# Kernel optimization log

Measured on AMD Instinct MI355X. Metric: run time of the kernel, lower is better.

Reference implementation:

```python
import jax, jax.numpy as jnp
import numpy as np

LOTRI2MAT = np.array([[0, 1, 3], [1, 2, 4], [3, 4, 5]])  # lower-tri 6-vec -> symmetric 3x3
MAT2LOTRI_I = np.array([0, 1, 1, 2, 2, 2])
MAT2LOTRI_J = np.array([0, 0, 1, 0, 1, 2])


def trilinear_warp_border(img, ddf):
    """MONAI Warp(mode='bilinear', padding_mode='border', align_corners=True).
    img: (B,C,H,W,D), ddf: (B,3,H,W,D) displacement in voxel units.
    Samples img at x + ddf(x), clamping coords to the volume (border padding).
    """
    B, C, H, W, D = img.shape
    base = jnp.stack(
        jnp.meshgrid(jnp.arange(H), jnp.arange(W), jnp.arange(D), indexing='ij'),
        axis=0,
    ).astype(img.dtype)  # (3,H,W,D)
    coords = ddf + base[None]  # (B,3,H,W,D)
    x = jnp.clip(coords[:, 0], 0.0, H - 1)
    y = jnp.clip(coords[:, 1], 0.0, W - 1)
    z = jnp.clip(coords[:, 2], 0.0, D - 1)

    x0f, y0f, z0f = jnp.floor(x), jnp.floor(y), jnp.floor(z)
    fx, fy, fz = x - x0f, y - y0f, z - z0f
    x0 = jnp.clip(x0f.astype(jnp.int32), 0, H - 1)
    y0 = jnp.clip(y0f.astype(jnp.int32), 0, W - 1)
    z0 = jnp.clip(z0f.astype(jnp.int32), 0, D - 1)
    x1 = jnp.minimum(x0 + 1, H - 1)
    y1 = jnp.minimum(y0 + 1, W - 1)
    z1 = jnp.minimum(z0 + 1, D - 1)

    def gather(img_b, xi, yi, zi):
        flat = (xi * W + yi) * D + zi  # (H,W,D)
        return img_b.reshape(C, -1)[:, flat.reshape(-1)].reshape(C, H, W, D)

    g = jax.vmap(gather)  # over batch

    out = jnp.zeros_like(img)
    for xi, wx in ((x0, 1.0 - fx), (x1, fx)):
        for yi, wy in ((y0, 1.0 - fy), (y1, fy)):
            for zi, wz in ((z0, 1.0 - fz), (z1, fz)):
                out = out + g(img, xi, yi, zi) * (wx * wy * wz)[:, None]
    return out


def jacobian_of_ddf(ddf):
    """J = I + du/dx via central differences (one-sided at boundaries).
    ddf: (B,3,H,W,D) -> (B,H,W,D,3,3) with J[...,i,j] = d u_i / d x_j + delta_ij."""
    grads = jnp.gradient(ddf, axis=(2, 3, 4))  # list over j of (B,3,H,W,D)
    J = jnp.stack(grads, axis=2)  # (B,3(i),3(j),H,W,D)
    J = J + jnp.eye(3, dtype=ddf.dtype)[None, :, :, None, None, None]
    return jnp.transpose(J, (0, 3, 4, 5, 1, 2))  # (B,H,W,D,3,3)


def setup_inputs() -> dict:
    key = jax.random.key(0)
    k1, k2 = jax.random.split(key)
    dti = jax.random.normal(k1, (2, 6, 64, 64, 64), dtype=jnp.float32)
    ddf = jax.random.normal(k2, (2, 3, 64, 64, 64), dtype=jnp.float32)
    return {"dti": dti, "ddf": ddf}


def reference(dti, ddf):
    b, _, h, w, d = dti.shape
    # 1) trilinear warp of the 6-channel lower-tri DTI
    dti_warped = trilinear_warp_border(dti, ddf)  # (B,6,H,W,D)
    # 2) lower-tri -> full symmetric 3x3, spatial-last
    M = dti_warped[:, LOTRI2MAT]                      # (B,3,3,H,W,D)
    M = jnp.transpose(M, (0, 3, 4, 5, 1, 2))          # (B,H,W,D,3,3)
    # 3) Jacobian of the deformation and its polar-decomposition rotation (finite strain)
    J = jacobian_of_ddf(ddf)                          # (B,H,W,D,3,3)
    U, _, Vh = jnp.linalg.svd(J, full_matrices=False)
    R = jnp.matmul(U, Vh)                             # orthogonal factor of J
    # 4) rotate tensors: R^T M R
    out = jnp.einsum('...ji,...jk,...kl->...il', R, M, R)
    # 5) back to lower-tri channel-first form
    out = jnp.transpose(out, (0, 4, 5, 1, 2, 3))      # (B,3,3,H,W,D)
    return out[:, MAT2LOTRI_I, MAT2LOTRI_J]           # (B,6,H,W,D)
```

## Files before the change

kernel.cpp:

```cpp
#include <hip/hip_runtime.h>

#define NVOX 262144
#define TOTAL (2 * NVOX)

typedef float f2u __attribute__((ext_vector_type(2), aligned(4)));

__global__ void zero_count(int* __restrict__ bad) {
    if (threadIdx.x == 0) bad[0] = 0;
}

__global__ __launch_bounds__(256)
void warp_main(const float* __restrict__ dti,
               const float* __restrict__ ddf,
               float* __restrict__ out,
               int* __restrict__ bad, int max_bad)
{
    const int idx = blockIdx.x * 256 + threadIdx.x;
    const int b = idx >> 18;
    const int r = idx & (NVOX - 1);
    const int x = r >> 12;
    const int y = (r >> 6) & 63;
    const int z = r & 63;

    const float* db = ddf + (size_t)b * 3 * NVOX;

    const float ux = db[r];
    const float uy = db[NVOX + r];
    const float uz = db[2 * NVOX + r];

    const float cx = fminf(fmaxf((float)x + ux, 0.0f), 63.0f);
    const float cy = fminf(fmaxf((float)y + uy, 0.0f), 63.0f);
    const float cz = fminf(fmaxf((float)z + uz, 0.0f), 63.0f);
    const float fx0 = floorf(cx), fy0 = floorf(cy), fz0 = floorf(cz);
    const float fx = cx - fx0, fy = cy - fy0, fz = cz - fz0;
    const int x0 = (int)fx0, y0 = (int)fy0, z0 = (int)fz0;
    const int x1 = min(x0 + 1, 63), y1 = min(y0 + 1, 63);

    const float gx = 1.0f - fx, gy = 1.0f - fy, gz = 1.0f - fz;
    const float q00 = gx * gy, q01 = gx * fy, q10 = fx * gy, q11 = fx * fy;

    const bool ztop = (z0 == 63);
    const int zb = ztop ? 62 : z0;
    const int p00 = (x0 * 64 + y0) * 64 + zb, p01 = (x0 * 64 + y1) * 64 + zb;
    const int p10 = (x1 * 64 + y0) * 64 + zb, p11 = (x1 * 64 + y1) * 64 + zb;

    const float* tb = dti + (size_t)b * 6 * NVOX;
    float m[6];
#pragma unroll
    for (int c = 0; c < 6; ++c) {
        const float* tc = tb + c * NVOX;
        const f2u v00 = *(const f2u*)(tc + p00);
        const f2u v01 = *(const f2u*)(tc + p01);
        const f2u v10 = *(const f2u*)(tc + p10);
        const f2u v11 = *(const f2u*)(tc + p11);
        const float l00 = (ztop ? v00.y : v00.x) * gz + v00.y * fz;
        const float l01 = (ztop ? v01.y : v01.x) * gz + v01.y * fz;
        const float l10 = (ztop ? v10.y : v10.x) * gz + v10.y * fz;
        const float l11 = (ztop ? v11.y : v11.x) * gz + v11.y * fz;
        m[c] = q00 * l00 + q01 * l01 + q10 * l10 + q11 * l11;
    }

    const int xm = max(x - 1, 0), xp = min(x + 1, 63);
    const int ym = max(y - 1, 0), yp = min(y + 1, 63);
    const int zm = max(z - 1, 0), zp = min(z + 1, 63);
    const float sx = (xp - xm == 2) ? 0.5f : 1.0f;
    const float sy = (yp - ym == 2) ? 0.5f : 1.0f;
    const float sz = (zp - zm == 2) ? 0.5f : 1.0f;

    float P[3][3];
#pragma unroll
    for (int i = 0; i < 3; ++i) {
        const float* ui = db + i * NVOX;
        const float ctr = (i == 0) ? ux : (i == 1) ? uy : uz;
        P[i][0] = (ui[(xp * 64 + y) * 64 + z] - ui[(xm * 64 + y) * 64 + z]) * sx
                + (i == 0 ? 1.0f : 0.0f);
        P[i][1] = (ui[(x * 64 + yp) * 64 + z] - ui[(x * 64 + ym) * 64 + z]) * sy
                + (i == 1 ? 1.0f : 0.0f);
        P[i][2] = (__shfl(ctr, zp) - __shfl(ctr, zm)) * sz + (i == 2 ? 1.0f : 0.0f);
    }

    float cond_est = 0.0f;
#pragma unroll
    for (int it = 0; it < 6; ++it) {
        const float C00 = P[1][1] * P[2][2] - P[1][2] * P[2][1];
        const float C01 = P[1][2] * P[2][0] - P[1][0] * P[2][2];
        const float C02 = P[1][0] * P[2][1] - P[1][1] * P[2][0];
        const float C10 = P[0][2] * P[2][1] - P[0][1] * P[2][2];
        const float C11 = P[0][0] * P[2][2] - P[0][2] * P[2][0];
        const float C12 = P[0][1] * P[2][0] - P[0][0] * P[2][1];
        const float C20 = P[0][1] * P[1][2] - P[0][2] * P[1][1];
        const float C21 = P[0][2] * P[1][0] - P[0][0] * P[1][2];
        const float C22 = P[0][0] * P[1][1] - P[0][1] * P[1][0];
        const float det = P[0][0] * C00 + P[0][1] * C01 + P[0][2] * C02;

        const float n2 = P[0][0]*P[0][0] + P[0][1]*P[0][1] + P[0][2]*P[0][2]
                       + P[1][0]*P[1][0] + P[1][1]*P[1][1] + P[1][2]*P[1][2]
                       + P[2][0]*P[2][0] + P[2][1]*P[2][1] + P[2][2]*P[2][2];
        const float a2 = C00*C00 + C01*C01 + C02*C02
                       + C10*C10 + C11*C11 + C12*C12
                       + C20*C20 + C21*C21 + C22*C22;

        const float ad = fmaxf(fabsf(det), 1e-30f);
        if (it == 0) cond_est = sqrtf(n2 * a2) / ad;

        const float t  = fmaxf(sqrtf(a2 / n2), 1e-20f);
        const float sg = (det < 0.0f) ? -1.0f : 1.0f;
        const float c1 = 0.5f * sqrtf(t / ad);
        const float c2 = 0.5f * sg / sqrtf(t * ad);

        P[0][0] = c1 * P[0][0] + c2 * C00;  P[0][1] = c1 * P[0][1] + c2 * C01;  P[0][2] = c1 * P[0][2] + c2 * C02;
        P[1][0] = c1 * P[1][0] + c2 * C10;  P[1][1] = c1 * P[1][1] + c2 * C11;  P[1][2] = c1 * P[1][2] + c2 * C12;
        P[2][0] = c1 * P[2][0] + c2 * C20;  P[2][1] = c1 * P[2][1] + c2 * C21;  P[2][2] = c1 * P[2][2] + c2 * C22;
    }

    const float M3[3][3] = {{m[0], m[1], m[3]},
                            {m[1], m[2], m[4]},
                            {m[3], m[4], m[5]}};
    float T[3][3];
#pragma unroll
    for (int i = 0; i < 3; ++i)
#pragma unroll
        for (int j = 0; j < 3; ++j)
            T[i][j] = P[0][i] * M3[0][j] + P[1][i] * M3[1][j] + P[2][i] * M3[2][j];

    float A[3][3];
#pragma unroll
    for (int i = 0; i < 3; ++i)
#pragma unroll
        for (int j = 0; j < 3; ++j)
            A[i][j] = T[i][0] * P[0][j] + T[i][1] * P[1][j] + T[i][2] * P[2][j];

    float* ob = out + (size_t)b * 6 * NVOX;
    ob[0 * NVOX + r] = A[0][0];
    ob[1 * NVOX + r] = A[1][0];
    ob[2 * NVOX + r] = A[1][1];
    ob[3 * NVOX + r] = A[2][0];
    ob[4 * NVOX + r] = A[2][1];
    ob[5 * NVOX + r] = A[2][2];

    if (cond_est > 1e4f) {
        const int slot = atomicAdd(bad, 1);
        if (slot < max_bad) bad[1 + slot] = idx;
    }
}

__global__ __launch_bounds__(256)
void rescue(const float* __restrict__ dti,
            const float* __restrict__ ddf,
            float* __restrict__ out,
            const int* __restrict__ bad, int max_bad)
{
    const int n = min(bad[0], max_bad);
    for (int k = blockIdx.x * 256 + threadIdx.x; k < n; k += 4 * 256) {
        const int idx = bad[1 + k];
        const int b = idx >> 18;
        const int r = idx & (NVOX - 1);
        const int x = r >> 12;
        const int y = (r >> 6) & 63;
        const int z = r & 63;

        const float* db = ddf + (size_t)b * 3 * NVOX;

        const float cx = fminf(fmaxf((float)x + db[r], 0.0f), 63.0f);
        const float cy = fminf(fmaxf((float)y + db[NVOX + r], 0.0f), 63.0f);
        const float cz = fminf(fmaxf((float)z + db[2 * NVOX + r], 0.0f), 63.0f);
        const float fx0 = floorf(cx), fy0 = floorf(cy), fz0 = floorf(cz);
        const float fx = cx - fx0, fy = cy - fy0, fz = cz - fz0;
        const int x0 = (int)fx0, y0 = (int)fy0, z0 = (int)fz0;
        const int x1 = min(x0 + 1, 63), y1 = min(y0 + 1, 63), z1 = min(z0 + 1, 63);
        const float gx = 1.0f - fx, gy = 1.0f - fy, gz = 1.0f - fz;
        const float w000 = gx*gy*gz, w001 = gx*gy*fz, w010 = gx*fy*gz, w011 = gx*fy*fz;
        const float w100 = fx*gy*gz, w101 = fx*gy*fz, w110 = fx*fy*gz, w111 = fx*fy*fz;
        const int o000 = (x0*64+y0)*64+z0, o001 = (x0*64+y0)*64+z1;
        const int o010 = (x0*64+y1)*64+z0, o011 = (x0*64+y1)*64+z1;
        const int o100 = (x1*64+y0)*64+z0, o101 = (x1*64+y0)*64+z1;
        const int o110 = (x1*64+y1)*64+z0, o111 = (x1*64+y1)*64+z1;

        const float* tb = dti + (size_t)b * 6 * NVOX;
        float m[6];
        for (int c = 0; c < 6; ++c) {
            const float* tc = tb + c * NVOX;
            m[c] = w000*tc[o000] + w001*tc[o001] + w010*tc[o010] + w011*tc[o011]
                 + w100*tc[o100] + w101*tc[o101] + w110*tc[o110] + w111*tc[o111];
        }

        const int xm = max(x-1,0), xp = min(x+1,63);
        const int ym = max(y-1,0), yp = min(y+1,63);
        const int zm = max(z-1,0), zp = min(z+1,63);
        const double sx = (xp-xm==2)?0.5:1.0, sy = (yp-ym==2)?0.5:1.0, sz = (zp-zm==2)?0.5:1.0;
        double X[3][3];
        for (int i = 0; i < 3; ++i) {
            const float* ui = db + i * NVOX;
            X[i][0] = ((double)ui[(xp*64+y)*64+z] - (double)ui[(xm*64+y)*64+z]) * sx + (i==0?1.0:0.0);
            X[i][1] = ((double)ui[(x*64+yp)*64+z] - (double)ui[(x*64+ym)*64+z]) * sy + (i==1?1.0:0.0);
            X[i][2] = ((double)ui[(x*64+y)*64+zp] - (double)ui[(x*64+y)*64+zm]) * sz + (i==2?1.0:0.0);
        }

        for (int it = 0; it < 14; ++it) {
            double mx = 0.0;
            for (int i = 0; i < 3; ++i)
                for (int j = 0; j < 3; ++j) mx = fmax(mx, fabs(X[i][j]));
            const double s = 1.0 / fmax(mx, 1e-300);
            for (int i = 0; i < 3; ++i)
                for (int j = 0; j < 3; ++j) X[i][j] *= s;

            const double C00 = X[1][1]*X[2][2] - X[1][2]*X[2][1];
            const double C01 = X[1][2]*X[2][0] - X[1][0]*X[2][2];
            const double C02 = X[1][0]*X[2][1] - X[1][1]*X[2][0];
            const double C10 = X[0][2]*X[2][1] - X[0][1]*X[2][2];
            const double C11 = X[0][0]*X[2][2] - X[0][2]*X[2][0];
            const double C12 = X[0][1]*X[2][0] - X[0][0]*X[2][1];
            const double C20 = X[0][1]*X[1][2] - X[0][2]*X[1][1];
            const double C21 = X[0][2]*X[1][0] - X[0][0]*X[1][2];
            const double C22 = X[0][0]*X[1][1] - X[0][1]*X[1][0];
            const double det = X[0][0]*C00 + X[0][1]*C01 + X[0][2]*C02;
            const double n2 = X[0][0]*X[0][0]+X[0][1]*X[0][1]+X[0][2]*X[0][2]
                            + X[1][0]*X[1][0]+X[1][1]*X[1][1]+X[1][2]*X[1][2]
                            + X[2][0]*X[2][0]+X[2][1]*X[2][1]+X[2][2]*X[2][2];
            const double a2 = C00*C00+C01*C01+C02*C02 + C10*C10+C11*C11+C12*C12
                            + C20*C20+C21*C21+C22*C22;
            const double t  = fmax(sqrt(a2 / n2), 1e-150);
            const double ad = fmax(fabs(det), 1e-280);
            const double sg = (det < 0.0) ? -1.0 : 1.0;
            const double c1 = 0.5 * sqrt(t / ad);
            const double c2 = 0.5 * sg / sqrt(t * ad);
            X[0][0]=c1*X[0][0]+c2*C00; X[0][1]=c1*X[0][1]+c2*C01; X[0][2]=c1*X[0][2]+c2*C02;
            X[1][0]=c1*X[1][0]+c2*C10; X[1][1]=c1*X[1][1]+c2*C11; X[1][2]=c1*X[1][2]+c2*C12;
            X[2][0]=c1*X[2][0]+c2*C20; X[2][1]=c1*X[2][1]+c2*C21; X[2][2]=c1*X[2][2]+c2*C22;
        }

        const double M3[3][3] = {{(double)m[0], (double)m[1], (double)m[3]},
                                 {(double)m[1], (double)m[2], (double)m[4]},
                                 {(double)m[3], (double)m[4], (double)m[5]}};
        double T[3][3], A[3][3];
        for (int i = 0; i < 3; ++i)
            for (int j = 0; j < 3; ++j)
                T[i][j] = X[0][i]*M3[0][j] + X[1][i]*M3[1][j] + X[2][i]*M3[2][j];
        for (int i = 0; i < 3; ++i)
            for (int j = 0; j < 3; ++j)
                A[i][j] = T[i][0]*X[0][j] + T[i][1]*X[1][j] + T[i][2]*X[2][j];

        float* ob = out + (size_t)b * 6 * NVOX;
        ob[0 * NVOX + r] = (float)A[0][0];
        ob[1 * NVOX + r] = (float)A[1][0];
        ob[2 * NVOX + r] = (float)A[1][1];
        ob[3 * NVOX + r] = (float)A[2][0];
        ob[4 * NVOX + r] = (float)A[2][1];
        ob[5 * NVOX + r] = (float)A[2][2];
    }
}

extern "C" void kernel_launch(void* const* d_in, const int* in_sizes, int n_in,
                              void* d_out, int out_size, void* d_ws, size_t ws_size,
                              hipStream_t stream) {
    const float* dti = (const float*)d_in[0];
    const float* ddf = (const float*)d_in[1];
    float* out = (float*)d_out;
    int* bad = (int*)d_ws;
    const int max_bad = (int)min((size_t)8192, ws_size / 4 - 1);

    zero_count<<<1, 64, 0, stream>>>(bad);
    warp_main<<<TOTAL / 256, 256, 0, stream>>>(dti, ddf, out, bad, max_bad);
    rescue<<<4, 256, 0, stream>>>(dti, ddf, out, bad, max_bad);
}
```

Measured before the change: 108.1 us.

## Replace atomic bad-list rescue with full-grid recheck kernel and fast math intrinsics

Drops the zero-count kernel and the atomic append of ill-conditioned voxels in the main kernel. A second full-grid kernel instead recomputes the Jacobian and condition estimate for every voxel and runs the double-precision polar iteration only where the estimate exceeds the threshold. The main kernel's Newton step now uses hardware rcp/rsq/sqrt intrinsics instead of IEEE divides and square roots. The trade is one fewer launch and no atomics, against a second full pass that rereads ddf for all 524K voxels, plus slightly less accurate float math.

After: 102.2 us. 1.06x faster.

```diff
diff --git a/kernel.cpp b/kernel.cpp
--- a/kernel.cpp
+++ b/kernel.cpp
@@ -4,16 +4,11 @@
 #define TOTAL (2 * NVOX)
 
 typedef float f2u __attribute__((ext_vector_type(2), aligned(4)));
-
-__global__ void zero_count(int* __restrict__ bad) {
-    if (threadIdx.x == 0) bad[0] = 0;
-}
 
 __global__ __launch_bounds__(256)
 void warp_main(const float* __restrict__ dti,
                const float* __restrict__ ddf,
-               float* __restrict__ out,
-               int* __restrict__ bad, int max_bad)
+               float* __restrict__ out)
 {
     const int idx = blockIdx.x * 256 + threadIdx.x;
     const int b = idx >> 18;
@@ -79,7 +74,6 @@
         P[i][2] = (__shfl(ctr, zp) - __shfl(ctr, zm)) * sz + (i == 2 ? 1.0f : 0.0f);
     }
 
-    float cond_est = 0.0f;
 #pragma unroll
     for (int it = 0; it < 6; ++it) {
         const float C00 = P[1][1] * P[2][2] - P[1][2] * P[2][1];
@@ -101,12 +95,11 @@
                        + C20*C20 + C21*C21 + C22*C22;
 
         const float ad = fmaxf(fabsf(det), 1e-30f);
-        if (it == 0) cond_est = sqrtf(n2 * a2) / ad;
-
-        const float t  = fmaxf(sqrtf(a2 / n2), 1e-20f);
+        const float t  = fmaxf(__builtin_amdgcn_sqrtf(a2 * __builtin_amdgcn_rcpf(n2)), 1e-20f);
         const float sg = (det < 0.0f) ? -1.0f : 1.0f;
-        const float c1 = 0.5f * sqrtf(t / ad);
-        const float c2 = 0.5f * sg / sqrtf(t * ad);
+        const float rt = __builtin_amdgcn_rsqf(t * ad);
+        const float c1 = 0.5f * t * rt;
+        const float c2 = 0.5f * sg * rt;
 
         P[0][0] = c1 * P[0][0] + c2 * C00;  P[0][1] = c1 * P[0][1] + c2 * C01;  P[0][2] = c1 * P[0][2] + c2 * C02;
         P[1][0] = c1 * P[1][0] + c2 * C10;  P[1][1] = c1 * P[1][1] + c2 * C11;  P[1][2] = c1 * P[1][2] + c2 * C12;
@@ -137,117 +130,140 @@
     ob[3 * NVOX + r] = A[2][0];
     ob[4 * NVOX + r] = A[2][1];
     ob[5 * NVOX + r] = A[2][2];
-
-    if (cond_est > 1e4f) {
-        const int slot = atomicAdd(bad, 1);
-        if (slot < max_bad) bad[1 + slot] = idx;
-    }
 }
 
 __global__ __launch_bounds__(256)
-void rescue(const float* __restrict__ dti,
-            const float* __restrict__ ddf,
-            float* __restrict__ out,
-            const int* __restrict__ bad, int max_bad)
+void rescue_all(const float* __restrict__ dti,
+                const float* __restrict__ ddf,
+                float* __restrict__ out)
 {
-    const int n = min(bad[0], max_bad);
-    for (int k = blockIdx.x * 256 + threadIdx.x; k < n; k += 4 * 256) {
-        const int idx = bad[1 + k];
-        const int b = idx >> 18;
-        const int r = idx & (NVOX - 1);
-        const int x = r >> 12;
-        const int y = (r >> 6) & 63;
-        const int z = r & 63;
-
-        const float* db = ddf + (size_t)b * 3 * NVOX;
-
-        const float cx = fminf(fmaxf((float)x + db[r], 0.0f), 63.0f);
-        const float cy = fminf(fmaxf((float)y + db[NVOX + r], 0.0f), 63.0f);
-        const float cz = fminf(fmaxf((float)z + db[2 * NVOX + r], 0.0f), 63.0f);
-        const float fx0 = floorf(cx), fy0 = floorf(cy), fz0 = floorf(cz);
-        const float fx = cx - fx0, fy = cy - fy0, fz = cz - fz0;
-        const int x0 = (int)fx0, y0 = (int)fy0, z0 = (int)fz0;
-        const int x1 = min(x0 + 1, 63), y1 = min(y0 + 1, 63), z1 = min(z0 + 1, 63);
-        const float gx = 1.0f - fx, gy = 1.0f - fy, gz = 1.0f - fz;
-        const float w000 = gx*gy*gz, w001 = gx*gy*fz, w010 = gx*fy*gz, w011 = gx*fy*fz;
-        const float w100 = fx*gy*gz, w101 = fx*gy*fz, w110 = fx*fy*gz, w111 = fx*fy*fz;
-        const int o000 = (x0*64+y0)*64+z0, o001 = (x0*64+y0)*64+z1;
-        const int o010 = (x0*64+y1)*64+z0, o011 = (x0*64+y1)*64+z1;
-        const int o100 = (x1*64+y0)*64+z0, o101 = (x1*64+y0)*64+z1;
-        const int o110 = (x1*64+y1)*64+z0, o111 = (x1*64+y1)*64+z1;
-
-        const float* tb = dti + (size_t)b * 6 * NVOX;
-        float m[6];
-        for (int c = 0; c < 6; ++c) {
-            const float* tc = tb + c * NVOX;
-            m[c] = w000*tc[o000] + w001*tc[o001] + w010*tc[o010] + w011*tc[o011]
-                 + w100*tc[o100] + w101*tc[o101] + w110*tc[o110] + w111*tc[o111];
-        }
-
-        const int xm = max(x-1,0), xp = min(x+1,63);
-        const int ym = max(y-1,0), yp = min(y+1,63);
-        const int zm = max(z-1,0), zp = min(z+1,63);
-        const double sx = (xp-xm==2)?0.5:1.0, sy = (yp-ym==2)?0.5:1.0, sz = (zp-zm==2)?0.5:1.0;
-        double X[3][3];
-        for (int i = 0; i < 3; ++i) {
-            const float* ui = db + i * NVOX;
-            X[i][0] = ((double)ui[(xp*64+y)*64+z] - (double)ui[(xm*64+y)*64+z]) * sx + (i==0?1.0:0.0);
-            X[i][1] = ((double)ui[(x*64+yp)*64+z] - (double)ui[(x*64+ym)*64+z]) * sy + (i==1?1.0:0.0);
-            X[i][2] = ((double)ui[(x*64+y)*64+zp] - (double)ui[(x*64+y)*64+zm]) * sz + (i==2?1.0:0.0);
-        }
-
-        for (int it = 0; it < 14; ++it) {
-            double mx = 0.0;
-            for (int i = 0; i < 3; ++i)
-                for (int j = 0; j < 3; ++j) mx = fmax(mx, fabs(X[i][j]));
-            const double s = 1.0 / fmax(mx, 1e-300);
-            for (int i = 0; i < 3; ++i)
-                for (int j = 0; j < 3; ++j) X[i][j] *= s;
-
-            const double C00 = X[1][1]*X[2][2] - X[1][2]*X[2][1];
-            const double C01 = X[1][2]*X[2][0] - X[1][0]*X[2][2];
-            const double C02 = X[1][0]*X[2][1] - X[1][1]*X[2][0];
-            const double C10 = X[0][2]*X[2][1] - X[0][1]*X[2][2];
-            const double C11 = X[0][0]*X[2][2] - X[0][2]*X[2][0];
-            const double C12 = X[0][1]*X[2][0] - X[0][0]*X[2][1];
-            const double C20 = X[0][1]*X[1][2] - X[0][2]*X[1][1];
-            const double C21 = X[0][2]*X[1][0] - X[0][0]*X[1][2];
-            const double C22 = X[0][0]*X[1][1] - X[0][1]*X[1][0];
-            const double det = X[0][0]*C00 + X[0][1]*C01 + X[0][2]*C02;
-            const double n2 = X[0][0]*X[0][0]+X[0][1]*X[0][1]+X[0][2]*X[0][2]
-                            + X[1][0]*X[1][0]+X[1][1]*X[1][1]+X[1][2]*X[1][2]
-                            + X[2][0]*X[2][0]+X[2][1]*X[2][1]+X[2][2]*X[2][2];
-            const double a2 = C00*C00+C01*C01+C02*C02 + C10*C10+C11*C11+C12*C12
-                            + C20*C20+C21*C21+C22*C22;
-            const double t  = fmax(sqrt(a2 / n2), 1e-150);
-            const double ad = fmax(fabs(det), 1e-280);
-            const double sg = (det < 0.0) ? -1.0 : 1.0;
-            const double c1 = 0.5 * sqrt(t / ad);
-            const double c2 = 0.5 * sg / sqrt(t * ad);
-            X[0][0]=c1*X[0][0]+c2*C00; X[0][1]=c1*X[0][1]+c2*C01; X[0][2]=c1*X[0][2]+c2*C02;
-            X[1][0]=c1*X[1][0]+c2*C10; X[1][1]=c1*X[1][1]+c2*C11; X[1][2]=c1*X[1][2]+c2*C12;
-            X[2][0]=c1*X[2][0]+c2*C20; X[2][1]=c1*X[2][1]+c2*C21; X[2][2]=c1*X[2][2]+c2*C22;
-        }
-
-        const double M3[3][3] = {{(double)m[0], (double)m[1], (double)m[3]},
-                                 {(double)m[1], (double)m[2], (double)m[4]},
-                                 {(double)m[3], (double)m[4], (double)m[5]}};
-        double T[3][3], A[3][3];
+    const int idx = blockIdx.x * 256 + threadIdx.x;
+    const int b = idx >> 18;
+    const int r = idx & (NVOX - 1);
+    const int x = r >> 12;
+    const int y = (r >> 6) & 63;
+    const int z = r & 63;
+
+    const float* db = ddf + (size_t)b * 3 * NVOX;
+
+    const int xm = max(x - 1, 0), xp = min(x + 1, 63);
+    const int ym = max(y - 1, 0), yp = min(y + 1, 63);
+    const int zm = max(z - 1, 0), zp = min(z + 1, 63);
+    const float sx = (xp - xm == 2) ? 0.5f : 1.0f;
+    const float sy = (yp - ym == 2) ? 0.5f : 1.0f;
+    const float sz = (zp - zm == 2) ? 0.5f : 1.0f;
+
+    float Jm[3][3];
+#pragma unroll
+    for (int i = 0; i < 3; ++i) {
+        const float* ui = db + i * NVOX;
+        Jm[i][0] = (ui[(xp * 64 + y) * 64 + z] - ui[(xm * 64 + y) * 64 + z]) * sx
+                 + (i == 0 ? 1.0f : 0.0f);
+        Jm[i][1] = (ui[(x * 64 + yp) * 64 + z] - ui[(x * 64 + ym) * 64 + z]) * sy
+                 + (i == 1 ? 1.0f : 0.0f);
+        Jm[i][2] = (ui[(x * 64 + y) * 64 + zp] - ui[(x * 64 + y) * 64 + zm]) * sz
+                 + (i == 2 ? 1.0f : 0.0f);
+    }
+
+    {
+        const float C00 = Jm[1][1]*Jm[2][2] - Jm[1][2]*Jm[2][1];
+        const float C01 = Jm[1][2]*Jm[2][0] - Jm[1][0]*Jm[2][2];
+        const float C02 = Jm[1][0]*Jm[2][1] - Jm[1][1]*Jm[2][0];
+        const float C10 = Jm[0][2]*Jm[2][1] - Jm[0][1]*Jm[2][2];
+        const float C11 = Jm[0][0]*Jm[2][2] - Jm[0][2]*Jm[2][0];
+        const float C12 = Jm[0][1]*Jm[2][0] - Jm[0][0]*Jm[2][1];
+        const float C20 = Jm[0][1]*Jm[1][2] - Jm[0][2]*Jm[1][1];
+        const float C21 = Jm[0][2]*Jm[1][0] - Jm[0][0]*Jm[1][2];
+        const float C22 = Jm[0][0]*Jm[1][1] - Jm[0][1]*Jm[1][0];
+        const float det = Jm[0][0]*C00 + Jm[0][1]*C01 + Jm[0][2]*C02;
+        const float n2 = Jm[0][0]*Jm[0][0]+Jm[0][1]*Jm[0][1]+Jm[0][2]*Jm[0][2]
+                       + Jm[1][0]*Jm[1][0]+Jm[1][1]*Jm[1][1]+Jm[1][2]*Jm[1][2]
+                       + Jm[2][0]*Jm[2][0]+Jm[2][1]*Jm[2][1]+Jm[2][2]*Jm[2][2];
+        const float a2 = C00*C00+C01*C01+C02*C02 + C10*C10+C11*C11+C12*C12
+                       + C20*C20+C21*C21+C22*C22;
+        const float ad = fmaxf(fabsf(det), 1e-30f);
+        const float ce = sqrtf(n2 * a2);
+        if (!(ce > 1e4f * ad)) return;
+    }
+
+    const float cx = fminf(fmaxf((float)x + db[r], 0.0f), 63.0f);
+    const float cy = fminf(fmaxf((float)y + db[NVOX + r], 0.0f), 63.0f);
+    const float cz = fminf(fmaxf((float)z + db[2 * NVOX + r], 0.0f), 63.0f);
+    const float fx0 = floorf(cx), fy0 = floorf(cy), fz0 = floorf(cz);
+    const float fx = cx - fx0, fy = cy - fy0, fz = cz - fz0;
+    const int x0 = (int)fx0, y0 = (int)fy0, z0 = (int)fz0;
+    const int x1 = min(x0 + 1, 63), y1 = min(y0 + 1, 63), z1 = min(z0 + 1, 63);
+    const float gx = 1.0f - fx, gy = 1.0f - fy, gz = 1.0f - fz;
+    const float w000 = gx*gy*gz, w001 = gx*gy*fz, w010 = gx*fy*gz, w011 = gx*fy*fz;
+    const float w100 = fx*gy*gz, w101 = fx*gy*fz, w110 = fx*fy*gz, w111 = fx*fy*fz;
+    const int o000 = (x0*64+y0)*64+z0, o001 = (x0*64+y0)*64+z1;
+    const int o010 = (x0*64+y1)*64+z0, o011 = (x0*64+y1)*64+z1;
+    const int o100 = (x1*64+y0)*64+z0, o101 = (x1*64+y0)*64+z1;
+    const int o110 = (x1*64+y1)*64+z0, o111 = (x1*64+y1)*64+z1;
+
+    const float* tb = dti + (size_t)b * 6 * NVOX;
+    float m[6];
+    for (int c = 0; c < 6; ++c) {
+        const float* tc = tb + c * NVOX;
+        m[c] = w000*tc[o000] + w001*tc[o001] + w010*tc[o010] + w011*tc[o011]
+             + w100*tc[o100] + w101*tc[o101] + w110*tc[o110] + w111*tc[o111];
+    }
+
+    double X[3][3];
+    for (int i = 0; i < 3; ++i)
+        for (int j = 0; j < 3; ++j) X[i][j] = (double)Jm[i][j];
+
+    for (int it = 0; it < 14; ++it) {
+        double mx = 0.0;
         for (int i = 0; i < 3; ++i)
-            for (int j = 0; j < 3; ++j)
-                T[i][j] = X[0][i]*M3[0][j] + X[1][i]*M3[1][j] + X[2][i]*M3[2][j];
+            for (int j = 0; j < 3; ++j) mx = fmax(mx, fabs(X[i][j]));
+        const double s = 1.0 / fmax(mx, 1e-300);
         for (int i = 0; i < 3; ++i)
-            for (int j = 0; j < 3; ++j)
-                A[i][j] = T[i][0]*X[0][j] + T[i][1]*X[1][j] + T[i][2]*X[2][j];
-
-        float* ob = out + (size_t)b * 6 * NVOX;
-        ob[0 * NVOX + r] = (float)A[0][0];
-        ob[1 * NVOX + r] = (float)A[1][0];
-        ob[2 * NVOX + r] = (float)A[1][1];
-        ob[3 * NVOX + r] = (float)A[2][0];
-        ob[4 * NVOX + r] = (float)A[2][1];
-        ob[5 * NVOX + r] = (float)A[2][2];
-    }
+            for (int j = 0; j < 3; ++j) X[i][j] *= s;
+
+        const double C00 = X[1][1]*X[2][2] - X[1][2]*X[2][1];
+        const double C01 = X[1][2]*X[2][0] - X[1][0]*X[2][2];
+        const double C02 = X[1][0]*X[2][1] - X[1][1]*X[2][0];
+        const double C10 = X[0][2]*X[2][1] - X[0][1]*X[2][2];
+        const double C11 = X[0][0]*X[2][2] - X[0][2]*X[2][0];
+        const double C12 = X[0][1]*X[2][0] - X[0][0]*X[2][1];
+        const double C20 = X[0][1]*X[1][2] - X[0][2]*X[1][1];
+        const double C21 = X[0][2]*X[1][0] - X[0][0]*X[1][2];
+        const double C22 = X[0][0]*X[1][1] - X[0][1]*X[1][0];
+        const double det = X[0][0]*C00 + X[0][1]*C01 + X[0][2]*C02;
+        const double n2 = X[0][0]*X[0][0]+X[0][1]*X[0][1]+X[0][2]*X[0][2]
+                        + X[1][0]*X[1][0]+X[1][1]*X[1][1]+X[1][2]*X[1][2]
+                        + X[2][0]*X[2][0]+X[2][1]*X[2][1]+X[2][2]*X[2][2];
+        const double a2 = C00*C00+C01*C01+C02*C02 + C10*C10+C11*C11+C12*C12
+                        + C20*C20+C21*C21+C22*C22;
+        const double t  = fmax(sqrt(a2 / n2), 1e-150);
+        const double ad = fmax(fabs(det), 1e-280);
+        const double sg = (det < 0.0) ? -1.0 : 1.0;
+        const double c1 = 0.5 * sqrt(t / ad);
+        const double c2 = 0.5 * sg / sqrt(t * ad);
+        X[0][0]=c1*X[0][0]+c2*C00; X[0][1]=c1*X[0][1]+c2*C01; X[0][2]=c1*X[0][2]+c2*C02;
+        X[1][0]=c1*X[1][0]+c2*C10; X[1][1]=c1*X[1][1]+c2*C11; X[1][2]=c1*X[1][2]+c2*C12;
+        X[2][0]=c1*X[2][0]+c2*C20; X[2][1]=c1*X[2][1]+c2*C21; X[2][2]=c1*X[2][2]+c2*C22;
+    }
+
+    const double M3[3][3] = {{(double)m[0], (double)m[1], (double)m[3]},
+                             {(double)m[1], (double)m[2], (double)m[4]},
+                             {(double)m[3], (double)m[4], (double)m[5]}};
+    double T[3][3], A[3][3];
+    for (int i = 0; i < 3; ++i)
+        for (int j = 0; j < 3; ++j)
+            T[i][j] = X[0][i]*M3[0][j] + X[1][i]*M3[1][j] + X[2][i]*M3[2][j];
+    for (int i = 0; i < 3; ++i)
+        for (int j = 0; j < 3; ++j)
+            A[i][j] = T[i][0]*X[0][j] + T[i][1]*X[1][j] + T[i][2]*X[2][j];
+
+    float* ob = out + (size_t)b * 6 * NVOX;
+    ob[0 * NVOX + r] = (float)A[0][0];
+    ob[1 * NVOX + r] = (float)A[1][0];
+    ob[2 * NVOX + r] = (float)A[1][1];
+    ob[3 * NVOX + r] = (float)A[2][0];
+    ob[4 * NVOX + r] = (float)A[2][1];
+    ob[5 * NVOX + r] = (float)A[2][2];
 }
 
 extern "C" void kernel_launch(void* const* d_in, const int* in_sizes, int n_in,
@@ -256,10 +272,8 @@
     const float* dti = (const float*)d_in[0];
     const float* ddf = (const float*)d_in[1];
     float* out = (float*)d_out;
-    int* bad = (int*)d_ws;
-    const int max_bad = (int)min((size_t)8192, ws_size / 4 - 1);
-
-    zero_count<<<1, 64, 0, stream>>>(bad);
-    warp_main<<<TOTAL / 256, 256, 0, stream>>>(dti, ddf, out, bad, max_bad);
-    rescue<<<4, 256, 0, stream>>>(dti, ddf, out, bad, max_bad);
+    (void)d_ws; (void)ws_size;
+
+    warp_main<<<TOTAL / 256, 256, 0, stream>>>(dti, ddf, out);
+    rescue_all<<<TOTAL / 256, 256, 0, stream>>>(dti, ddf, out);
 }
```
